# Kernel tuning notes

Hardware: AMD Instinct MI355X
Metric: run time of the kernel (lower is better)

Reference implementation:

```python
import jax, jax.numpy as jnp
import numpy as np

# ---- static module configuration ----
N_POU = 16
N_BC = 3
P = N_POU + N_BC          # full_n_pou = 19
F = 3                      # n_fields
B, N, D_IN, D_Z, D_H = 16, 1024, 32, 64, 64
N_DIR = 64
MAX_ITERS = 50
ALPHA = 0.1                # damped fixed-point step of the nonlinear solver

# edge_pairs / delta_0 for the complete graph on P POU nodes (construct_delta0)
_ei, _ej = np.triu_indices(P, 1)
E = _ei.shape[0]           # n_one_forms = P*(P-1)/2 = 171
_d0 = np.zeros((E, P), np.float32)
_d0[np.arange(E), _ei] = -1.0
_d0[np.arange(E), _ej] = 1.0
DELTA0 = jnp.asarray(_d0)  # [E, P]
EI = jnp.asarray(_ei)
EJ = jnp.asarray(_ej)


def setup_inputs() -> dict:
    key = jax.random.key(0)
    ks = jax.random.split(key, 16)
    f32 = jnp.float32
    inp = {
        'in_tokens': jax.random.normal(ks[0], (B, N, D_IN), f32),
        'K_list': 0.02 * jax.random.normal(ks[1], (B, F, N, N), f32),
        'M_list': 0.02 * jax.random.normal(ks[2], (B, F, N, N), f32),
        'dirichlet_nodes': jax.random.randint(ks[3], (B, N_DIR), 0, N),
        'boundary_vals': jax.random.normal(ks[4], (B, N_DIR, F), f32),
        'u_init': jax.random.normal(ks[5], (B, P * F), f32),
        # learned parameters (encoder / source_model / boundary_w / flux_model)
        'W_enc': jax.random.normal(ks[6], (D_IN, D_Z), f32) / np.sqrt(D_IN),
        'b_enc': jnp.zeros((D_Z,), f32),
        'W_src': jax.random.normal(ks[7], (D_Z, F), f32) / np.sqrt(D_Z),
        'b_src': jnp.zeros((F,), f32),
        'W_pou': jax.random.normal(ks[8], (D_Z, P * F), f32) / np.sqrt(D_Z),
        'Wf1': jax.random.normal(ks[9], (2 * F, D_H), f32) / np.sqrt(2 * F),
        'Wz': jax.random.normal(ks[10], (D_Z, D_H), f32) / np.sqrt(D_Z),
        'bf': jnp.zeros((D_H,), f32),
        'Wf2': 0.1 * jax.random.normal(ks[11], (D_H, F), f32) / np.sqrt(D_H),
    }
    return inp


def reference(in_tokens, K_list, M_list, dirichlet_nodes, boundary_vals, u_init,
              W_enc, b_enc, W_src, b_src, W_pou, Wf1, Wz, bf, Wf2):
    Bc, Nn = in_tokens.shape[0], in_tokens.shape[1]
    latent_scaling = Nn / P

    # encoder: in_tokens -> per-node latents z [B,N,Dz]
    z = jnp.tanh(in_tokens @ W_enc + b_enc)

    # boundary_w: partition-of-unity weights W [B,P,N,F], boundary POUs biased
    # toward Dirichlet nodes via boundary_vals
    logits = (z @ W_pou).reshape(Bc, Nn, P, F)
    bidx = jnp.arange(Bc)[:, None]
    bvals_full = jnp.zeros((Bc, Nn, F), in_tokens.dtype).at[bidx, dirichlet_nodes].set(boundary_vals)
    logits = logits.at[:, :, P - N_BC:, :].add(bvals_full[:, :, None, :])
    Wmat = jax.nn.softmax(logits, axis=2).transpose(0, 2, 1, 3)  # [B,P,N,F]

    # source_model + latent projection (source_mode='identity' -> pass-through)
    f_full = z @ W_src + b_src                                    # [B,N,F]
    f_latent = jnp.einsum('bpif,bif->bpf', Wmat, f_full) / latent_scaling

    # project_bilinear_per_field: K_hat[b,p,q,f] = W K W^T / scaling
    def project(Kl):
        t = jnp.einsum('bpif,bfij->bpjf', Wmat, Kl)               # [B,P,N,F]
        return jnp.einsum('bpjf,bqjf->bpqf', t, Wmat) / latent_scaling

    # apply_dirichlet_per_field: boundary rows -> identity
    eyeP = jnp.eye(P, dtype=in_tokens.dtype)
    row_mask = jnp.zeros((P,), bool).at[P - N_BC:].set(True)
    def dirichlet_bilinear(Kh):
        return jnp.where(row_mask[None, :, None, None], eyeP[None, :, :, None], Kh)

    K_hat = dirichlet_bilinear(project(K_list))                   # [B,P,P,F]
    M_hat = dirichlet_bilinear(project(M_list))

    bc_mask = jnp.zeros((P, F), bool).at[P - N_BC:, :].set(True)
    bc_vals = jnp.zeros((P, F), in_tokens.dtype).at[P - N_BC, :].set(1.0)

    # flux_model conditioning: pooled latent, precomputed once
    zp = jnp.mean(z, axis=1) @ Wz                                 # [B,Dh]
    src_term = jnp.einsum('bpqf,bqf->bpf', M_hat, f_latent)       # constant in u

    def G(u_flat):  # G_residual
        u = u_flat.reshape(Bc, P, F)
        diff_term = jnp.einsum('bpqf,bqf->bpf', K_hat, u)
        ue = jnp.concatenate([u[:, EI], u[:, EJ]], axis=-1)       # [B,E,2F]
        flux = jnp.tanh(ue @ Wf1 + zp[:, None, :] + bf) @ Wf2     # [B,E,F]
        flux_term = jnp.einsum('ep,bef->bpf', DELTA0, flux)
        r = diff_term - src_term - flux_term
        r = jnp.where(bc_mask[None], u - bc_vals[None], r)        # Dirichlet residual
        return r.reshape(Bc, -1)

    # NonlinearSolver: damped fixed-point iteration, fixed MAX_ITERS under jit
    def step(u, _):
        return u - ALPHA * G(u), None
    u_hat, _ = jax.lax.scan(step, u_init, None, length=MAX_ITERS)

    u_coarse = u_hat.reshape(Bc, P, F)
    u_fine = jnp.einsum('bpif,bpf->bif', Wmat, u_coarse)          # [B,N,F]
    return u_fine
```

## Files before the change

### kernel.cpp

```cpp
#include <hip/hip_runtime.h>

#define Bn 16
#define Nn 1024
#define DIN 32
#define DZ 64
#define Fc 3
#define Pp 19
#define PPAD 20
#define Ee 171
#define ITERS 50
#define INV_SCALE (19.0f/1024.0f)
#define CHUNK 64
#define PF 4
#define PFK 8

#define OFF_WPROJ 0
#define OFF_FFULL 983040
#define OFF_FLAT  1033216
#define OFF_UBUF  1034128
#define OFF_BVALS 1035040
#define OFF_ZACC  1084192
#define OFF_KHAT  1085216
#define OFF_SRC   1099808
#define ZERO_FLOATS 65536
#define OFF_TPART 1100576
#define NEED_FLOATS (OFF_TPART + 48*16*16*1024)

__global__ __launch_bounds__(1024) void k_scatter(const int* __restrict__ nodes,
                                                  const float* __restrict__ bvals,
                                                  float* __restrict__ bfull) {
  __shared__ int sn[1024];
  int tid = threadIdx.x;
  sn[tid] = nodes[tid];
  __syncthreads();
  int b = tid >> 6, j = tid & 63;
  int node = sn[tid];
  bool win = true;
  for (int j2 = j + 1; j2 < 64; j2++)
    if (sn[(b << 6) | j2] == node) { win = false; break; }
  if (win) {
    #pragma unroll
    for (int f = 0; f < Fc; f++)
      bfull[((size_t)b*Nn + node)*Fc + f] = bvals[(size_t)tid*Fc + f];
  }
}

__global__ __launch_bounds__(128) void k_encode(
    const float* __restrict__ x, const float* __restrict__ Wenc, const float* __restrict__ benc,
    const float* __restrict__ Wsrc, const float* __restrict__ bsrc, const float* __restrict__ Wpou,
    const float* __restrict__ bfull, float* __restrict__ wproj, float* __restrict__ ffull,
    float* __restrict__ zacc) {
  __shared__ float sWenc[DIN*DZ];
  __shared__ float sWpou[DZ*57];
  __shared__ float sWsrc[DZ*Fc];
  int tid = threadIdx.x;
  for (int t = tid; t < DIN*DZ; t += 128) sWenc[t] = Wenc[t];
  for (int t = tid; t < DZ*57; t += 128) sWpou[t] = Wpou[t];
  for (int t = tid; t < DZ*Fc; t += 128) sWsrc[t] = Wsrc[t];
  __syncthreads();
  int g = blockIdx.x*128 + tid;
  int b = g >> 10, i = g & 1023;
  float xr[DIN];
  const float* xp = x + (size_t)g*DIN;
  #pragma unroll
  for (int k = 0; k < DIN; k += 4) {
    float4 t4 = *(const float4*)(xp + k);
    xr[k] = t4.x; xr[k+1] = t4.y; xr[k+2] = t4.z; xr[k+3] = t4.w;
  }
  float l[57];
  #pragma unroll
  for (int o = 0; o < 57; o++) l[o] = 0.f;
  float ff[3] = {bsrc[0], bsrc[1], bsrc[2]};
  int lane = tid & 63;
  for (int d = 0; d < DZ; d++) {
    float zd = benc[d];
    #pragma unroll
    for (int k = 0; k < DIN; k++) zd = fmaf(xr[k], sWenc[k*DZ + d], zd);
    zd = tanhf(zd);
    #pragma unroll
    for (int o = 0; o < 57; o++) l[o] = fmaf(zd, sWpou[d*57 + o], l[o]);
    #pragma unroll
    for (int f = 0; f < Fc; f++) ff[f] = fmaf(zd, sWsrc[d*Fc + f], ff[f]);
    float zs = zd;
    #pragma unroll
    for (int off = 32; off > 0; off >>= 1) zs += __shfl_xor(zs, off, 64);
    if (lane == 0) atomicAdd(&zacc[b*DZ + d], zs);
  }
  #pragma unroll
  for (int f = 0; f < Fc; f++) ffull[(size_t)g*Fc + f] = ff[f];
  #pragma unroll
  for (int f = 0; f < Fc; f++) {
    float bv = bfull[(size_t)g*Fc + f];
    l[16*3+f] += bv; l[17*3+f] += bv; l[18*3+f] += bv;
  }
  #pragma unroll
  for (int f = 0; f < Fc; f++) {
    float m = l[f];
    #pragma unroll
    for (int p = 1; p < Pp; p++) m = fmaxf(m, l[p*3+f]);
    float ex[Pp]; float s = 0.f;
    #pragma unroll
    for (int p = 0; p < Pp; p++) { ex[p] = __expf(l[p*3+f] - m); s += ex[p]; }
    float inv = 1.f / s;
    float* wp = wproj + ((size_t)(b*Fc + f)*Nn + i)*PPAD;
    #pragma unroll
    for (int p = 0; p < Pp; p++) wp[p] = ex[p]*inv;
  }
}

__global__ __launch_bounds__(256) void k_flat(const float* __restrict__ wproj,
                                              const float* __restrict__ ffull,
                                              float* __restrict__ flat) {
  int bf = blockIdx.x;
  int b = bf / 3, f = bf % 3;
  float acc[Pp];
  #pragma unroll
  for (int q = 0; q < Pp; q++) acc[q] = 0.f;
  for (int i = threadIdx.x; i < Nn; i += 256) {
    float fv = ffull[((size_t)b*Nn + i)*Fc + f];
    const float* row = wproj + ((size_t)bf*Nn + i)*PPAD;
    #pragma unroll
    for (int q = 0; q < Pp; q++) acc[q] = fmaf(row[q], fv, acc[q]);
  }
  #pragma unroll
  for (int q = 0; q < Pp; q++) {
    float v = acc[q];
    #pragma unroll
    for (int off = 32; off > 0; off >>= 1) v += __shfl_xor(v, off, 64);
    acc[q] = v;
  }
  __shared__ float red[4][Pp];
  int wave = threadIdx.x >> 6, lane = threadIdx.x & 63;
  if (lane == 0) {
    #pragma unroll
    for (int q = 0; q < Pp; q++) red[wave][q] = acc[q];
  }
  __syncthreads();
  if (threadIdx.x < Pp) {
    float s = red[0][threadIdx.x] + red[1][threadIdx.x] + red[2][threadIdx.x] + red[3][threadIdx.x];
    flat[bf*Pp + threadIdx.x] = s * INV_SCALE;
  }
}

__global__ __launch_bounds__(256, 3) void k_projT(
    const float* __restrict__ Kl, const float* __restrict__ wproj,
    float* __restrict__ tpart) {
  __shared__ float sW[16*CHUNK];
  int chunk = blockIdx.x;
  int bf = blockIdx.y;
  int i0 = chunk * CHUNK;
  const float* Kb = Kl + (size_t)bf*Nn*Nn + (size_t)i0*Nn;
  const float* Wrow0 = wproj + ((size_t)bf*Nn + i0)*PPAD;
  int tid = threadIdx.x;
  for (int t = tid; t < 16*CHUNK; t += 256) {
    int r = t & (CHUNK-1), p = t >> 6;
    sW[p*CHUNK + r] = Wrow0[r*PPAD + p];
  }
  __syncthreads();
  int j0 = tid * 4;
  float4 acc[16];
  #pragma unroll
  for (int p = 0; p < 16; p++) { acc[p].x = 0.f; acc[p].y = 0.f; acc[p].z = 0.f; acc[p].w = 0.f; }
  const float* kp = Kb + j0;
  float4 kbuf[PFK];
  #pragma unroll
  for (int s = 0; s < PFK; s++) kbuf[s] = *(const float4*)(kp + (size_t)s*Nn);
  for (int ii = 0; ii < CHUNK; ii += PFK) {
    #pragma unroll
    for (int s = 0; s < PFK; s++) {
      float4 k4 = kbuf[s];
      int nxt = (ii + PFK + s) & (CHUNK - 1);
      kbuf[s] = *(const float4*)(kp + (size_t)nxt*Nn);
      const float* wrow = &sW[ii + s];
      #pragma unroll
      for (int p = 0; p < 16; p++) {
        float wv = wrow[p*CHUNK];
        acc[p].x = fmaf(wv, k4.x, acc[p].x);
        acc[p].y = fmaf(wv, k4.y, acc[p].y);
        acc[p].z = fmaf(wv, k4.z, acc[p].z);
        acc[p].w = fmaf(wv, k4.w, acc[p].w);
      }
    }
  }
  float* tp = tpart + ((size_t)(bf*16 + chunk)*16)*Nn + j0;
  #pragma unroll
  for (int p = 0; p < 16; p++) *(float4*)(tp + (size_t)p*Nn) = acc[p];
}

__global__ __launch_bounds__(256, 3) void k_projM(
    const float* __restrict__ Ml, const float* __restrict__ wproj,
    const float* __restrict__ flat, float* __restrict__ srca) {
  __shared__ float sW[16*CHUNK];
  int chunk = blockIdx.x;
  int bf = blockIdx.y;
  int i0 = chunk * CHUNK;
  const float* Mb = Ml + (size_t)bf*Nn*Nn + (size_t)i0*Nn;
  const float* Wp = wproj + (size_t)bf*Nn*PPAD;
  const float* Wrow0 = Wp + (size_t)i0*PPAD;
  int tid = threadIdx.x;
  for (int t = tid; t < 16*CHUNK; t += 256) {
    int r = t & (CHUNK-1), p = t >> 6;
    sW[p*CHUNK + r] = Wrow0[r*PPAD + p];
  }
  float fl[Pp];
  #pragma unroll
  for (int q = 0; q < Pp; q++) fl[q] = flat[bf*Pp + q];
  int j0 = tid * 4;
  float v0, v1, v2, v3;
  {
    float vv[4];
    #pragma unroll
    for (int r = 0; r < 4; r++) {
      const float* row = Wp + (size_t)(j0 + r)*PPAD;
      float s = 0.f;
      #pragma unroll
      for (int q = 0; q < Pp; q++) s = fmaf(row[q], fl[q], s);
      vv[r] = s;
    }
    v0 = vv[0]; v1 = vv[1]; v2 = vv[2]; v3 = vv[3];
  }
  __syncthreads();
  float sa[16];
  #pragma unroll
  for (int p = 0; p < 16; p++) sa[p] = 0.f;
  const float* mp = Mb + j0;
  float4 mbuf[PFK];
  #pragma unroll
  for (int s = 0; s < PFK; s++) mbuf[s] = *(const float4*)(mp + (size_t)s*Nn);
  for (int ii = 0; ii < CHUNK; ii += PFK) {
    #pragma unroll
    for (int s = 0; s < PFK; s++) {
      float4 m4 = mbuf[s];
      int nxt = (ii + PFK + s) & (CHUNK - 1);
      mbuf[s] = *(const float4*)(mp + (size_t)nxt*Nn);
      float tm = m4.x*v0 + m4.y*v1 + m4.z*v2 + m4.w*v3;
      const float* wrow = &sW[ii + s];
      #pragma unroll
      for (int p = 0; p < 16; p++) sa[p] = fmaf(wrow[p*CHUNK], tm, sa[p]);
    }
  }
  int lane = tid & 63;
  #pragma unroll
  for (int p = 0; p < 16; p++) {
    float vq = sa[p];
    #pragma unroll
    for (int off = 32; off > 0; off >>= 1) vq += __shfl_xor(vq, off, 64);
    sa[p] = vq;
  }
  if (lane == 0) {
    #pragma unroll
    for (int p = 0; p < 16; p++) atomicAdd(&srca[bf*16 + p], sa[p] * INV_SCALE);
  }
}

__global__ __launch_bounds__(256) void k_khat(const float* __restrict__ tpart,
                                              const float* __restrict__ wproj,
                                              float* __restrict__ khat) {
  __shared__ float sT[16*64];
  __shared__ float sWq[64*PPAD];
  int jb = blockIdx.x, bf = blockIdx.y;
  int tid = threadIdx.x;
  {
    int id = tid * 4;
    int p = id >> 6;
    int r = id & 63;
    const float* base = tpart + ((size_t)(bf*16)*16 + p)*Nn + jb*64 + r;
    float4 s4 = make_float4(0.f, 0.f, 0.f, 0.f);
    #pragma unroll 4
    for (int c = 0; c < 16; c++) {
      float4 t4 = *(const float4*)(base + (size_t)c*16*Nn);
      s4.x += t4.x; s4.y += t4.y; s4.z += t4.z; s4.w += t4.w;
    }
    *(float4*)&sT[p*64 + r] = s4;
  }
  const float* wsrc = wproj + ((size_t)bf*Nn + jb*64)*PPAD;
  for (int t = tid; t < 64*PPAD; t += 256) sWq[t] = wsrc[t];
  __syncthreads();
  for (int o = tid; o < 16*Pp; o += 256) {
    int p = o / Pp, q = o - p*Pp;
    float s = 0.f;
    #pragma unroll
    for (int r = 0; r < 64; r++) s = fmaf(sT[p*64 + r], sWq[r*PPAD + q], s);
    atomicAdd(&khat[(bf*16 + p)*Pp + q], s * INV_SCALE);
  }
}

__global__ __launch_bounds__(256, 1) void k_project_fb(
    const float* __restrict__ Kl, const float* __restrict__ Ml,
    const float* __restrict__ wproj, const float* __restrict__ flat,
    float* __restrict__ khat, float* __restrict__ srca) {
  __shared__ float sW[16*CHUNK];
  int chunk = blockIdx.x;
  int bf = blockIdx.y;
  int i0 = chunk * CHUNK;
  const float* Kb = Kl + (size_t)bf*Nn*Nn + (size_t)i0*Nn;
  const float* Mb = Ml + (size_t)bf*Nn*Nn + (size_t)i0*Nn;
  const float* Wp = wproj + (size_t)bf*Nn*PPAD;
  const float* Wrow0 = Wp + (size_t)i0*PPAD;
  int tid = threadIdx.x;
  for (int t = tid; t < 16*CHUNK; t += 256) {
    int r = t & (CHUNK-1), p = t >> 6;
    sW[p*CHUNK + r] = Wrow0[r*PPAD + p];
  }
  float fl[Pp];
  #pragma unroll
  for (int q = 0; q < Pp; q++) fl[q] = flat[bf*Pp + q];
  int j0 = tid * 4;
  float v[4];
  #pragma unroll
  for (int r = 0; r < 4; r++) {
    const float* row = Wp + (size_t)(j0 + r)*PPAD;
    float s = 0.f;
    #pragma unroll
    for (int q = 0; q < Pp; q++) s = fmaf(row[q], fl[q], s);
    v[r] = s;
  }
  __syncthreads();
  float4 acc[16];
  float sa[16];
  #pragma unroll
  for (int p = 0; p < 16; p++) {
    acc[p].x = 0.f; acc[p].y = 0.f; acc[p].z = 0.f; acc[p].w = 0.f;
    sa[p] = 0.f;
  }
  const float* kp = Kb + j0;
  const float* mp = Mb + j0;
  float4 kbuf[PF], mbuf[PF];
  #pragma unroll
  for (int s = 0; s < PF; s++) {
    kbuf[s] = *(const float4*)(kp + (size_t)s*Nn);
    mbuf[s] = *(const float4*)(mp + (size_t)s*Nn);
  }
  for (int ii = 0; ii < CHUNK; ii += PF) {
    #pragma unroll
    for (int s = 0; s < PF; s++) {
      float4 k4 = kbuf[s], m4 = mbuf[s];
      int nxt = (ii + PF + s) & (CHUNK - 1);
      kbuf[s] = *(const float4*)(kp + (size_t)nxt*Nn);
      mbuf[s] = *(const float4*)(mp + (size_t)nxt*Nn);
      float tm = m4.x*v[0] + m4.y*v[1] + m4.z*v[2] + m4.w*v[3];
      const float* wrow = &sW[ii + s];
      #pragma unroll
      for (int p = 0; p < 16; p++) {
        float wv = wrow[p*CHUNK];
        acc[p].x = fmaf(wv, k4.x, acc[p].x);
        acc[p].y = fmaf(wv, k4.y, acc[p].y);
        acc[p].z = fmaf(wv, k4.z, acc[p].z);
        acc[p].w = fmaf(wv, k4.w, acc[p].w);
        sa[p] = fmaf(wv, tm, sa[p]);
      }
    }
  }
  int lane = tid & 63;
  #pragma unroll
  for (int q = 0; q < Pp; q++) {
    float w0 = Wp[(size_t)(j0 + 0)*PPAD + q];
    float w1 = Wp[(size_t)(j0 + 1)*PPAD + q];
    float w2 = Wp[(size_t)(j0 + 2)*PPAD + q];
    float w3 = Wp[(size_t)(j0 + 3)*PPAD + q];
    float pr[16];
    #pragma unroll
    for (int p = 0; p < 16; p++)
      pr[p] = acc[p].x*w0 + acc[p].y*w1 + acc[p].z*w2 + acc[p].w*w3;
    #pragma unroll
    for (int p = 0; p < 16; p++) {
      float vq = pr[p];
      #pragma unroll
      for (int off = 32; off > 0; off >>= 1) vq += __shfl_xor(vq, off, 64);
      pr[p] = vq;
    }
    if (lane == 0) {
      #pragma unroll
      for (int p = 0; p < 16; p++)
        atomicAdd(&khat[(bf*16 + p)*Pp + q], pr[p] * INV_SCALE);
    }
  }
  #pragma unroll
  for (int p = 0; p < 16; p++) {
    float vq = sa[p];
    #pragma unroll
    for (int off = 32; off > 0; off >>= 1) vq += __shfl_xor(vq, off, 64);
    sa[p] = vq;
  }
  if (lane == 0) {
    #pragma unroll
    for (int p = 0; p < 16; p++) atomicAdd(&srca[bf*16 + p], sa[p] * INV_SCALE);
  }
}

#define ABS 65
__global__ __launch_bounds__(704, 1) void k_solve(
    const float* __restrict__ khat, const float* __restrict__ srca,
    const float* __restrict__ zacc, const float* __restrict__ Wz,
    const float* __restrict__ u_init, const float* __restrict__ Wf1,
    const float* __restrict__ bfv, const float* __restrict__ Wf2,
    float* __restrict__ ubuf) {
  int b = blockIdx.x;
  __shared__ float u_s[57];
  __shared__ float flux_s[Ee*Fc];
  __shared__ float sW1[6*DZ];
  __shared__ float sW2[DZ*Fc];
  __shared__ float sbz[DZ];
  __shared__ float sK[Fc*16*Pp];
  __shared__ float ssrc[Fc*16];
  __shared__ float sA[Pp*ABS];
  __shared__ float sB[Pp*ABS];
  int tid = threadIdx.x;
  for (int t = tid; t < 6*DZ; t += 704) sW1[t] = Wf1[t];
  for (int t = tid; t < DZ*Fc; t += 704) sW2[t] = Wf2[t];
  if (tid < DZ) {
    float s = 0.f;
    for (int k = 0; k < DZ; k++) s = fmaf(zacc[b*DZ + k], Wz[k*DZ + tid], s);
    sbz[tid] = bfv[tid] + s * (1.f/1024.f);
  }
  for (int t = tid; t < Fc*16*Pp; t += 704) sK[t] = khat[b*Fc*16*Pp + t];
  if (tid < 48) ssrc[tid] = srca[b*48 + tid];
  if (tid < 57) u_s[tid] = u_init[b*57 + tid];
  __syncthreads();
  int e = tid >> 2, h = tid & 3;
  bool active = (tid < 4*Ee);
  int ei = 0, ej = 0;
  if (active) {
    int r = e, i = 0;
    while (r >= 18 - i) { r -= 18 - i; i++; }
    ei = i; ej = i + 1 + r;
  }
  int d0 = h * 16;
  bool upd = (tid < 57);
  int up = 0, uf = 0;
  if (upd) { up = tid / 3; uf = tid % 3; }
  for (int it = 0; it < ITERS; it++) {
    for (int t = tid; t < 2*Pp*DZ; t += 704) {
      int half = (t >= Pp*DZ);
      int t2 = half ? t - Pp*DZ : t;
      int p = t2 >> 6, d = t2 & 63;
      const float* w1 = sW1 + (half ? 3*DZ : 0) + d;
      float s = u_s[p*3+0]*w1[0] + u_s[p*3+1]*w1[DZ] + u_s[p*3+2]*w1[2*DZ];
      (half ? sB : sA)[p*ABS + d] = s;
    }
    __syncthreads();
    if (active) {
      const float* Ap = sA + ei*ABS;
      const float* Bp = sB + ej*ABS;
      float fl0 = 0.f, fl1 = 0.f, fl2 = 0.f;
      for (int dd = 0; dd < 16; dd++) {
        int d = d0 + dd;
        float pre = sbz[d] + Ap[d] + Bp[d];
        float xc = fminf(fmaxf(pre, -20.f), 20.f);
        float t = __expf(2.f * xc);
        float th = (t - 1.f) / (t + 1.f);
        fl0 = fmaf(th, sW2[d*3 + 0], fl0);
        fl1 = fmaf(th, sW2[d*3 + 1], fl1);
        fl2 = fmaf(th, sW2[d*3 + 2], fl2);
      }
      fl0 += __shfl_xor(fl0, 1, 64); fl0 += __shfl_xor(fl0, 2, 64);
      fl1 += __shfl_xor(fl1, 1, 64); fl1 += __shfl_xor(fl1, 2, 64);
      fl2 += __shfl_xor(fl2, 1, 64); fl2 += __shfl_xor(fl2, 2, 64);
      if (h == 0) { flux_s[e*3+0] = fl0; flux_s[e*3+1] = fl1; flux_s[e*3+2] = fl2; }
    }
    __syncthreads();
    if (upd) {
      int p = up, f = uf;
      float u_old = u_s[tid];
      float r_;
      if (p < 16) {
        float diff = 0.f;
        for (int q = 0; q < Pp; q++) diff = fmaf(sK[(f*16 + p)*Pp + q], u_s[q*3 + f], diff);
        float ft = 0.f;
        for (int o = 0; o < Pp; o++) {
          if (o == p) continue;
          int i_ = (o < p) ? o : p;
          int j_ = (o < p) ? p : o;
          int eidx = i_*Pp - (i_*(i_+1))/2 + (j_ - i_ - 1);
          float sgn = (o < p) ? 1.f : -1.f;
          ft += sgn * flux_s[eidx*3 + f];
        }
        r_ = diff - ssrc[f*16 + p] - ft;
      } else {
        r_ = u_old - ((p == 16) ? 1.f : 0.f);
      }
      u_s[tid] = u_old - 0.1f * r_;
    }
    __syncthreads();
  }
  if (tid < 57) ubuf[b*57 + tid] = u_s[tid];
}

__global__ __launch_bounds__(256) void k_out(const float* __restrict__ wproj,
                                             const float* __restrict__ ubuf,
                                             float* __restrict__ out) {
  __shared__ float u_s[57];
  int b = blockIdx.y;
  int i = blockIdx.x*256 + threadIdx.x;
  if (threadIdx.x < 57) u_s[threadIdx.x] = ubuf[b*57 + threadIdx.x];
  __syncthreads();
  #pragma unroll
  for (int f = 0; f < Fc; f++) {
    const float* row = wproj + ((size_t)(b*Fc + f)*Nn + i)*PPAD;
    float s = 0.f;
    #pragma unroll
    for (int p = 0; p < Pp; p++) s = fmaf(row[p], u_s[p*3 + f], s);
    out[((size_t)b*Nn + i)*Fc + f] = s;
  }
}

extern "C" void kernel_launch(void* const* d_in, const int* in_sizes, int n_in,
                              void* d_out, int out_size, void* d_ws, size_t ws_size,
                              hipStream_t stream) {
  const float* in_tokens = (const float*)d_in[0];
  const float* K_list    = (const float*)d_in[1];
  const float* M_list    = (const float*)d_in[2];
  const int*   dnodes    = (const int*)d_in[3];
  const float* bvals     = (const float*)d_in[4];
  const float* u_init    = (const float*)d_in[5];
  const float* W_enc     = (const float*)d_in[6];
  const float* b_enc     = (const float*)d_in[7];
  const float* W_src     = (const float*)d_in[8];
  const float* b_src     = (const float*)d_in[9];
  const float* W_pou     = (const float*)d_in[10];
  const float* Wf1       = (const float*)d_in[11];
  const float* Wz        = (const float*)d_in[12];
  const float* bfv       = (const float*)d_in[13];
  const float* Wf2       = (const float*)d_in[14];
  float* ws  = (float*)d_ws;
  float* out = (float*)d_out;

  float* WPROJ = ws + OFF_WPROJ;
  float* FFULL = ws + OFF_FFULL;
  float* FLAT  = ws + OFF_FLAT;
  float* UBUF  = ws + OFF_UBUF;
  float* BVALS = ws + OFF_BVALS;
  float* ZACC  = ws + OFF_ZACC;
  float* KHAT  = ws + OFF_KHAT;
  float* SRC   = ws + OFF_SRC;
  float* TPART = ws + OFF_TPART;

  hipMemsetAsync(ws + OFF_BVALS, 0, (size_t)ZERO_FLOATS * sizeof(float), stream);
  k_scatter<<<1, 1024, 0, stream>>>(dnodes, bvals, BVALS);
  k_encode<<<128, 128, 0, stream>>>(in_tokens, W_enc, b_enc, W_src, b_src, W_pou,
                                    BVALS, WPROJ, FFULL, ZACC);
  k_flat<<<Bn*Fc, 256, 0, stream>>>(WPROJ, FFULL, FLAT);
  if (ws_size >= (size_t)NEED_FLOATS * sizeof(float)) {
    k_projT<<<dim3(Nn/CHUNK, Bn*Fc), 256, 0, stream>>>(K_list, WPROJ, TPART);
    k_projM<<<dim3(Nn/CHUNK, Bn*Fc), 256, 0, stream>>>(M_list, WPROJ, FLAT, SRC);
    k_khat<<<dim3(16, Bn*Fc), 256, 0, stream>>>(TPART, WPROJ, KHAT);
  } else {
    k_project_fb<<<dim3(Nn/CHUNK, Bn*Fc), 256, 0, stream>>>(K_list, M_list, WPROJ, FLAT, KHAT, SRC);
  }
  k_solve<<<Bn, 704, 0, stream>>>(KHAT, SRC, ZACC, Wz, u_init, Wf1, bfv, Wf2, UBUF);
  k_out<<<dim3(Nn/256, Bn), 256, 0, stream>>>(WPROJ, UBUF, out);
}
```

Baseline: 748.3 us.

## Fuse per-node projection into edge flux loop and shrink solve block

Removes the separate per-iteration projection stage (sA/sB) and its extra barrier. Each edge thread now computes its pre-activation directly from packed u and weight vectors, using float4 LDS loads. The tanh is rewritten as 1-2/(exp(2x)+1) with a hardware reciprocal and with the factor 2 folded into the weights. Threads drop from 704 to 384, with 2 threads per edge instead of 4. This cuts one sync per iteration of the serial 50-step loop, but gives each thread more redundant FMA work.

New measurement: 787.7 us. 1.05x slower.

```diff
diff --git a/kernel.cpp b/kernel.cpp
--- a/kernel.cpp
+++ b/kernel.cpp
@@ -388,102 +388,107 @@
   }
 }
 
-#define ABS 65
-__global__ __launch_bounds__(704, 1) void k_solve(
+__global__ __launch_bounds__(384, 1) void k_solve(
     const float* __restrict__ khat, const float* __restrict__ srca,
     const float* __restrict__ zacc, const float* __restrict__ Wz,
     const float* __restrict__ u_init, const float* __restrict__ Wf1,
     const float* __restrict__ bfv, const float* __restrict__ Wf2,
     float* __restrict__ ubuf) {
   int b = blockIdx.x;
-  __shared__ float u_s[57];
+  __shared__ float u4[Pp*4];
   __shared__ float flux_s[Ee*Fc];
-  __shared__ float sW1[6*DZ];
-  __shared__ float sW2[DZ*Fc];
-  __shared__ float sbz[DZ];
+  __shared__ float sW1p[DZ*8];
+  __shared__ float sW2p[DZ*4];
   __shared__ float sK[Fc*16*Pp];
   __shared__ float ssrc[Fc*16];
-  __shared__ float sA[Pp*ABS];
-  __shared__ float sB[Pp*ABS];
-  int tid = threadIdx.x;
-  for (int t = tid; t < 6*DZ; t += 704) sW1[t] = Wf1[t];
-  for (int t = tid; t < DZ*Fc; t += 704) sW2[t] = Wf2[t];
+  int tid = threadIdx.x;
+  for (int t = tid; t < 6*DZ; t += 384) {
+    int k = t >> 6, d = t & 63;
+    sW1p[d*8 + k] = 2.f * Wf1[t];
+  }
+  for (int t = tid; t < DZ*Fc; t += 384) {
+    int d = t / 3, c = t - d*3;
+    sW2p[d*4 + c] = Wf2[t];
+  }
   if (tid < DZ) {
     float s = 0.f;
     for (int k = 0; k < DZ; k++) s = fmaf(zacc[b*DZ + k], Wz[k*DZ + tid], s);
-    sbz[tid] = bfv[tid] + s * (1.f/1024.f);
-  }
-  for (int t = tid; t < Fc*16*Pp; t += 704) sK[t] = khat[b*Fc*16*Pp + t];
+    sW1p[tid*8 + 6] = 2.f * (bfv[tid] + s * (1.f/1024.f));
+    sW1p[tid*8 + 7] = 0.f;
+    sW2p[tid*4 + 3] = 0.f;
+  }
+  for (int t = tid; t < Fc*16*Pp; t += 384) sK[t] = khat[b*Fc*16*Pp + t];
   if (tid < 48) ssrc[tid] = srca[b*48 + tid];
-  if (tid < 57) u_s[tid] = u_init[b*57 + tid];
-  __syncthreads();
-  int e = tid >> 2, h = tid & 3;
-  bool active = (tid < 4*Ee);
+  if (tid < 57) u4[(tid/3)*4 + (tid%3)] = u_init[b*57 + tid];
+  if (tid < Pp) u4[tid*4 + 3] = 0.f;
+  __syncthreads();
+  int e = tid >> 1, h = tid & 1;
+  bool active = (e < Ee);
   int ei = 0, ej = 0;
   if (active) {
     int r = e, i = 0;
     while (r >= 18 - i) { r -= 18 - i; i++; }
     ei = i; ej = i + 1 + r;
   }
-  int d0 = h * 16;
+  int d0 = h * 32;
   bool upd = (tid < 57);
-  int up = 0, uf = 0;
-  if (upd) { up = tid / 3; uf = tid % 3; }
+  int up = tid / 3, uf = tid - (tid/3)*3;
   for (int it = 0; it < ITERS; it++) {
-    for (int t = tid; t < 2*Pp*DZ; t += 704) {
-      int half = (t >= Pp*DZ);
-      int t2 = half ? t - Pp*DZ : t;
-      int p = t2 >> 6, d = t2 & 63;
-      const float* w1 = sW1 + (half ? 3*DZ : 0) + d;
-      float s = u_s[p*3+0]*w1[0] + u_s[p*3+1]*w1[DZ] + u_s[p*3+2]*w1[2*DZ];
-      (half ? sB : sA)[p*ABS + d] = s;
-    }
-    __syncthreads();
     if (active) {
-      const float* Ap = sA + ei*ABS;
-      const float* Bp = sB + ej*ABS;
+      float4 ua = *(const float4*)&u4[ei*4];
+      float4 ub = *(const float4*)&u4[ej*4];
       float fl0 = 0.f, fl1 = 0.f, fl2 = 0.f;
-      for (int dd = 0; dd < 16; dd++) {
+      #pragma unroll 16
+      for (int dd = 0; dd < 32; dd++) {
         int d = d0 + dd;
-        float pre = sbz[d] + Ap[d] + Bp[d];
-        float xc = fminf(fmaxf(pre, -20.f), 20.f);
-        float t = __expf(2.f * xc);
-        float th = (t - 1.f) / (t + 1.f);
-        fl0 = fmaf(th, sW2[d*3 + 0], fl0);
-        fl1 = fmaf(th, sW2[d*3 + 1], fl1);
-        fl2 = fmaf(th, sW2[d*3 + 2], fl2);
+        float4 wA = *(const float4*)&sW1p[d*8];
+        float4 wB = *(const float4*)&sW1p[d*8 + 4];
+        float pre = wB.z;
+        pre = fmaf(ua.x, wA.x, pre);
+        pre = fmaf(ua.y, wA.y, pre);
+        pre = fmaf(ua.z, wA.z, pre);
+        pre = fmaf(ub.x, wA.w, pre);
+        pre = fmaf(ub.y, wB.x, pre);
+        pre = fmaf(ub.z, wB.y, pre);
+        float t = __expf(pre);
+        float r = __builtin_amdgcn_rcpf(t + 1.f);
+        float th = fmaf(-2.f, r, 1.f);
+        float4 w2 = *(const float4*)&sW2p[d*4];
+        fl0 = fmaf(th, w2.x, fl0);
+        fl1 = fmaf(th, w2.y, fl1);
+        fl2 = fmaf(th, w2.z, fl2);
       }
-      fl0 += __shfl_xor(fl0, 1, 64); fl0 += __shfl_xor(fl0, 2, 64);
-      fl1 += __shfl_xor(fl1, 1, 64); fl1 += __shfl_xor(fl1, 2, 64);
-      fl2 += __shfl_xor(fl2, 1, 64); fl2 += __shfl_xor(fl2, 2, 64);
+      fl0 += __shfl_xor(fl0, 1, 64);
+      fl1 += __shfl_xor(fl1, 1, 64);
+      fl2 += __shfl_xor(fl2, 1, 64);
       if (h == 0) { flux_s[e*3+0] = fl0; flux_s[e*3+1] = fl1; flux_s[e*3+2] = fl2; }
     }
     __syncthreads();
     if (upd) {
-      int p = up, f = uf;
-      float u_old = u_s[tid];
+      float u_old = u4[up*4 + uf];
       float r_;
-      if (p < 16) {
+      if (up < 16) {
         float diff = 0.f;
-        for (int q = 0; q < Pp; q++) diff = fmaf(sK[(f*16 + p)*Pp + q], u_s[q*3 + f], diff);
+        const float* kr = &sK[(uf*16 + up)*Pp];
+        for (int q = 0; q < Pp; q++) diff = fmaf(kr[q], u4[q*4 + uf], diff);
         float ft = 0.f;
         for (int o = 0; o < Pp; o++) {
-          if (o == p) continue;
-          int i_ = (o < p) ? o : p;
-          int j_ = (o < p) ? p : o;
+          if (o == up) continue;
+          int i_ = (o < up) ? o : up;
+          int j_ = (o < up) ? up : o;
           int eidx = i_*Pp - (i_*(i_+1))/2 + (j_ - i_ - 1);
-          float sgn = (o < p) ? 1.f : -1.f;
-          ft += sgn * flux_s[eidx*3 + f];
+          float sgn = (o < up) ? 1.f : -1.f;
+          ft += sgn * flux_s[eidx*3 + uf];
         }
-        r_ = diff - ssrc[f*16 + p] - ft;
+        r_ = diff - ssrc[uf*16 + up] - ft;
       } else {
-        r_ = u_old - ((p == 16) ? 1.f : 0.f);
+        r_ = u_old - ((up == 16) ? 1.f : 0.f);
       }
-      u_s[tid] = u_old - 0.1f * r_;
+      u4[up*4 + uf] = u_old - 0.1f * r_;
     }
     __syncthreads();
   }
-  if (tid < 57) ubuf[b*57 + tid] = u_s[tid];
+  if (tid < 57) ubuf[b*57 + tid] = u4[(tid/3)*4 + (tid%3)];
 }
 
 __global__ __launch_bounds__(256) void k_out(const float* __restrict__ wproj,
@@ -547,6 +552,6 @@
   } else {
     k_project_fb<<<dim3(Nn/CHUNK, Bn*Fc), 256, 0, stream>>>(K_list, M_list, WPROJ, FLAT, KHAT, SRC);
   }
-  k_solve<<<Bn, 704, 0, stream>>>(KHAT, SRC, ZACC, Wz, u_init, Wf1, bfv, Wf2, UBUF);
+  k_solve<<<Bn, 384, 0, stream>>>(KHAT, SRC, ZACC, Wz, u_init, Wf1, bfv, Wf2, UBUF);
   k_out<<<dim3(Nn/256, Bn), 256, 0, stream>>>(WPROJ, UBUF, out);
 }
```
